# Kernel tuning notes

Hardware: AMD Instinct MI355X
Metric: run time of the kernel (lower is better)

The kernel has to match this reference:

```python
import jax, jax.numpy as jnp
import numpy as np

BOX_WARP = 1.0
TRIPLANE_DEPTH = 1
PLANES = jnp.array([[[1, 0, 0], [0, 1, 0], [0, 0, 1]],
                    [[1, 0, 0], [0, 0, 1], [0, 1, 0]],
                    [[0, 1, 0], [0, 0, 1], [1, 0, 0]]], dtype=jnp.float32)
INV_PLANES = jnp.linalg.inv(PLANES)  # [3,3,3]


def project_onto_planes(coords):
    # coords [N,M,3] -> projections [N*3, M, 3] (bmm with inverse plane axes)
    N, M, _ = coords.shape
    proj = jnp.einsum('nmc,pcd->npmd', coords, INV_PLANES)
    return proj.reshape(N * 3, M, 3)


def grid_sample_3d(feat, grid):
    # torch.nn.functional.grid_sample 5D, mode=bilinear(trilinear), padding_mode=zeros,
    # align_corners=False. feat [B,C,D,H,W], grid [B,M,3] with (x->W, y->H, z->D).
    B, C, D, H, W = feat.shape
    x = ((grid[..., 0] + 1.0) * W - 1.0) * 0.5
    y = ((grid[..., 1] + 1.0) * H - 1.0) * 0.5
    z = ((grid[..., 2] + 1.0) * D - 1.0) * 0.5
    x0f = jnp.floor(x); y0f = jnp.floor(y); z0f = jnp.floor(z)
    wx = x - x0f; wy = y - y0f; wz = z - z0f
    x0 = x0f.astype(jnp.int32); y0 = y0f.astype(jnp.int32); z0 = z0f.astype(jnp.int32)
    feat_flat = feat.reshape(B, C, D * H * W)

    def corner(zi, yi, xi, w):
        valid = ((zi >= 0) & (zi < D) & (yi >= 0) & (yi < H) & (xi >= 0) & (xi < W))
        idx = (jnp.clip(zi, 0, D - 1) * H + jnp.clip(yi, 0, H - 1)) * W + jnp.clip(xi, 0, W - 1)
        v = jnp.take_along_axis(feat_flat, idx[:, None, :], axis=2)  # [B,C,M]
        return v * (w * valid)[:, None, :]

    out = (corner(z0, y0, x0, (1 - wz) * (1 - wy) * (1 - wx))
           + corner(z0, y0, x0 + 1, (1 - wz) * (1 - wy) * wx)
           + corner(z0, y0 + 1, x0, (1 - wz) * wy * (1 - wx))
           + corner(z0, y0 + 1, x0 + 1, (1 - wz) * wy * wx)
           + corner(z0 + 1, y0, x0, wz * (1 - wy) * (1 - wx))
           + corner(z0 + 1, y0, x0 + 1, wz * (1 - wy) * wx)
           + corner(z0 + 1, y0 + 1, x0, wz * wy * (1 - wx))
           + corner(z0 + 1, y0 + 1, x0 + 1, wz * wy * wx))
    return out  # [B,C,M]


def sample_from_planes(plane_feats_list, coordinates):
    N, M, _ = coordinates.shape
    proj = project_onto_planes(coordinates * (2.0 / BOX_WARP))  # [N*3,M,3]
    out = None
    for pf in plane_feats_list:
        _, P, CD, H, W = pf.shape
        C = CD // TRIPLANE_DEPTH
        f = pf.reshape(N * 3, C, TRIPLANE_DEPTH, H, W)
        s = grid_sample_3d(f, proj)  # [N*3,C,M]
        s = s.reshape(N, 3, C, M).transpose(0, 1, 3, 2)  # [N,3,M,C]
        out = s if out is None else out + s
    return out / len(plane_feats_list)


def ray_march(colors, densities, depths):
    # MipRayMarcher2 (EG3D): midpoint sampling, softplus(d-1) activation, alpha compositing.
    deltas = depths[:, :, 1:] - depths[:, :, :-1]                    # [N,R,S-1,1]
    cmid = 0.5 * (colors[:, :, :-1] + colors[:, :, 1:])
    dmid = 0.5 * (densities[:, :, :-1] + densities[:, :, 1:])
    dmid = jax.nn.softplus(dmid - 1.0)
    alpha = 1.0 - jnp.exp(-dmid * deltas)                            # [N,R,S-1,1]
    shifted = jnp.concatenate([jnp.ones_like(alpha[:, :, :1]), 1.0 - alpha + 1e-10], axis=2)
    weights = alpha * jnp.cumprod(shifted, axis=2)[:, :, :-1]
    rgb = jnp.sum(weights * cmid, axis=2)                            # [N,R,3]
    return rgb


def setup_inputs() -> dict:
    key = jax.random.key(0)
    ks = jax.random.split(key, 6)
    N, C = 4, 32
    R, S = 4096, 48
    M = R * S
    plane_lo = jax.random.normal(ks[0], (N, 3, C, 256, 256), jnp.float32) * 0.1
    plane_hi = jax.random.normal(ks[1], (N, 3, C, 512, 512), jnp.float32) * 0.1
    coordinates = jax.random.uniform(ks[2], (N, M, 3), jnp.float32, -0.45, 0.45)
    depths = 2.25 + 1.2 * jnp.sort(jax.random.uniform(ks[3], (N, R, S, 1), jnp.float32), axis=2)
    w_sigma = jax.random.normal(ks[4], (C, 1), jnp.float32) * 0.1
    w_rgb = jax.random.normal(ks[5], (C, 3), jnp.float32) * 0.1
    return {"plane_lo": plane_lo, "plane_hi": plane_hi, "coordinates": coordinates,
            "depths": depths, "w_sigma": w_sigma, "w_rgb": w_rgb}


def reference(plane_lo, plane_hi, coordinates, depths, w_sigma, w_rgb):
    N, R, S, _ = depths.shape
    feats = sample_from_planes([plane_lo, plane_hi], coordinates).mean(axis=1)  # [N,M,C]
    sigma = feats @ w_sigma                                                      # [N,M,1]
    rgb = jax.nn.sigmoid(feats @ w_rgb)                                          # [N,M,3]
    return ray_march(rgb.reshape(N, R, S, 3), sigma.reshape(N, R, S, 1), depths)
```

## Files before the change

### kernel.cpp

```cpp
#include <hip/hip_runtime.h>
#include <hip/hip_bf16.h>
#include <cstdint>

#define N_IMG 4
#define C_CH 32
#define R_RAYS 4096
#define S_SAMP 48
#define M_PTS (R_RAYS * S_SAMP)

typedef float f32x4 __attribute__((ext_vector_type(4)));
typedef unsigned int u32x4 __attribute__((ext_vector_type(4)));

__device__ __forceinline__ unsigned f2bf(float f) {
  __hip_bfloat16 h = __float2bfloat16(f);
  return (unsigned)*reinterpret_cast<unsigned short*>(&h);
}
__device__ __forceinline__ float bflo(unsigned u) { return __uint_as_float(u << 16); }
__device__ __forceinline__ float bfhi(unsigned u) { return __uint_as_float(u & 0xffff0000u); }

#define LO_BLOCKS 768
#define HI_BLOCKS 3072

__global__ __launch_bounds__(256) void project_planes(
    const float* __restrict__ lo, const float* __restrict__ hi,
    const float* __restrict__ w_sigma, const float* __restrict__ w_rgb,
    uint4* __restrict__ lo_out, uint4* __restrict__ hi_out) {
  __shared__ float sw[4 * C_CH];
  int t = threadIdx.x;
  if (t < C_CH) sw[t * 4] = w_sigma[t];
  if (t < 3 * C_CH) sw[(t / 3) * 4 + 1 + (t % 3)] = w_rgb[t];
  __syncthreads();

  int bid = blockIdx.x;
  const float* in;
  uint4* out;
  int logW, g, c0, c1;
  if (bid < LO_BLOCKS) {
    in = lo; out = lo_out; logW = 8; g = bid * 256 + t; c0 = 11; c1 = 244;
  } else {
    in = hi; out = hi_out; logW = 9; g = (bid - LO_BLOCKS) * 256 + t; c0 = 24; c1 = 488;
  }
  int W = 1 << logW;
  int hw = (g * 4) & ((W * W) - 1);
  int np = (g * 4) >> (2 * logW);
  int h = hw >> logW, w = hw & (W - 1);
  if (h < c0 || h > c1 || (w + 3) < c0 || w > c1) return;

  const float* base = in + ((size_t)np << (5 + 2 * logW)) + hw;
  f32x4 as = 0.f, ar = 0.f, ag = 0.f, ab = 0.f;
#pragma unroll
  for (int c = 0; c < C_CH; ++c) {
    f32x4 f;
    __builtin_memcpy(&f, base + ((size_t)c << (2 * logW)), 16);
    as += f * sw[c * 4 + 0];
    ar += f * sw[c * 4 + 1];
    ag += f * sw[c * 4 + 2];
    ab += f * sw[c * 4 + 3];
  }
  uint4 o0, o1;
  o0.x = f2bf(as.x) | (f2bf(ar.x) << 16);
  o0.y = f2bf(ag.x) | (f2bf(ab.x) << 16);
  o0.z = f2bf(as.y) | (f2bf(ar.y) << 16);
  o0.w = f2bf(ag.y) | (f2bf(ab.y) << 16);
  o1.x = f2bf(as.z) | (f2bf(ar.z) << 16);
  o1.y = f2bf(ag.z) | (f2bf(ab.z) << 16);
  o1.z = f2bf(as.w) | (f2bf(ar.w) << 16);
  o1.w = f2bf(ag.w) | (f2bf(ab.w) << 16);
  out[g * 2 + 0] = o0;
  out[g * 2 + 1] = o1;
}

__global__ __launch_bounds__(256) void gather_pts(
    const float* __restrict__ coords,
    const uint2* __restrict__ lo_p,
    const uint2* __restrict__ hi_p,
    float4* __restrict__ pts)
{
  int idx = blockIdx.x * 256 + threadIdx.x;
  int n = idx / M_PTS;

  float X = coords[idx * 3 + 0] * 2.f;
  float Y = coords[idx * 3 + 1] * 2.f;
  float Z = coords[idx * 3 + 2] * 2.f;

  float acc0 = 0.f, acc1 = 0.f, acc2 = 0.f, acc3 = 0.f;
  const float gxs[3] = {X, X, Y};
  const float gys[3] = {Y, Z, Z};
  const float gzs[3] = {Z, Y, X};

#pragma unroll
  for (int p = 0; p < 3; ++p) {
    float wz = (1.f - 0.5f * fabsf(gzs[p])) * (1.f / 6.f);
#pragma unroll
    for (int lev = 0; lev < 2; ++lev) {
      const int logW = lev ? 9 : 8;
      const int W = 1 << logW;
      const uint2* pl = lev ? hi_p : lo_p;
      float xf = ((gxs[p] + 1.f) * (float)W - 1.f) * 0.5f;
      float yf = ((gys[p] + 1.f) * (float)W - 1.f) * 0.5f;
      float x0f = floorf(xf), y0f = floorf(yf);
      float fx = xf - x0f, fy = yf - y0f;
      int x0 = (int)x0f, y0 = (int)y0f;
      x0 = min(max(x0, 0), W - 2);
      y0 = min(max(y0, 0), W - 2);
      int base = ((((n * 3 + p) << logW) + y0) << logW) + x0;
      u32x4 r0, r1;
      __builtin_memcpy(&r0, pl + base, 16);
      __builtin_memcpy(&r1, pl + base + W, 16);
      float w00 = wz * (1.f - fy) * (1.f - fx);
      float w01 = wz * (1.f - fy) * fx;
      float w10 = wz * fy * (1.f - fx);
      float w11 = wz * fy * fx;
      acc0 += w00 * bflo(r0.x) + w01 * bflo(r0.z) + w10 * bflo(r1.x) + w11 * bflo(r1.z);
      acc1 += w00 * bfhi(r0.x) + w01 * bfhi(r0.z) + w10 * bfhi(r1.x) + w11 * bfhi(r1.z);
      acc2 += w00 * bflo(r0.y) + w01 * bflo(r0.w) + w10 * bflo(r1.y) + w11 * bflo(r1.w);
      acc3 += w00 * bfhi(r0.y) + w01 * bfhi(r0.w) + w10 * bfhi(r1.y) + w11 * bfhi(r1.w);
    }
  }

  float4 o;
  o.x = 1.f / (1.f + __expf(-acc1));
  o.y = 1.f / (1.f + __expf(-acc2));
  o.z = 1.f / (1.f + __expf(-acc3));
  o.w = acc0;
  pts[idx] = o;
}

__global__ __launch_bounds__(256) void ray_march_k(
    const float4* __restrict__ pts, const float* __restrict__ depths,
    float* __restrict__ out) {
  int t = blockIdx.x * 256 + threadIdx.x;
  const float4* p = pts + (size_t)t * S_SAMP;
  const float* d = depths + (size_t)t * S_SAMP;

  float4 prev = p[0];
  float dprev = d[0];
  float T = 1.f, accR = 0.f, accG = 0.f, accB = 0.f;
#pragma unroll 4
  for (int i = 1; i < S_SAMP; ++i) {
    float4 cur = p[i];
    float dcur = d[i];
    float delta = dcur - dprev;
    float cr = 0.5f * (prev.x + cur.x);
    float cg = 0.5f * (prev.y + cur.y);
    float cb = 0.5f * (prev.z + cur.z);
    float dm = 0.5f * (prev.w + cur.w) - 1.f;
    float sp = fmaxf(dm, 0.f) + log1pf(__expf(-fabsf(dm)));
    float a = 1.f - __expf(-sp * delta);
    float w = a * T;
    accR += w * cr; accG += w * cg; accB += w * cb;
    T *= (1.f - a + 1e-10f);
    prev = cur; dprev = dcur;
  }
  out[t * 3 + 0] = accR;
  out[t * 3 + 1] = accG;
  out[t * 3 + 2] = accB;
}

extern "C" void kernel_launch(void* const* d_in, const int* in_sizes, int n_in,
                              void* d_out, int out_size, void* d_ws, size_t ws_size,
                              hipStream_t stream) {
  const float* plane_lo = (const float*)d_in[0];
  const float* plane_hi = (const float*)d_in[1];
  const float* coords   = (const float*)d_in[2];
  const float* depths   = (const float*)d_in[3];
  const float* w_sigma  = (const float*)d_in[4];
  const float* w_rgb    = (const float*)d_in[5];

  const size_t LO_TEX = (size_t)12 * 256 * 256;
  const size_t HI_TEX = (size_t)12 * 512 * 512;
  char* ws = (char*)d_ws;
  uint2* lo_p = (uint2*)ws;
  uint2* hi_p = (uint2*)(ws + LO_TEX * 8);
  float4* pts = (float4*)(ws + (LO_TEX + HI_TEX) * 8);

  project_planes<<<LO_BLOCKS + HI_BLOCKS, 256, 0, stream>>>(
      plane_lo, plane_hi, w_sigma, w_rgb, (uint4*)lo_p, (uint4*)hi_p);

  gather_pts<<<(N_IMG * M_PTS) / 256, 256, 0, stream>>>(
      coords, lo_p, hi_p, pts);

  ray_march_k<<<(N_IMG * R_RAYS) / 256, 256, 0, stream>>>(
      pts, depths, (float*)d_out);
}
```

Measured before the change: 180.2 us.

## Split point gather into per-level passes with bf16 intermediate

Splits the gather kernel into a low-resolution pass and a high-resolution pass, so each pass touches only one projected texture. The partial sums go through a bf16 workspace buffer. Each pass processes two points per thread, uses nontemporal loads and stores, and interleaves blocks across images. The ray-march block size drops to 64 so more CUs get work. This adds an extra intermediate write and read, reads the coordinates twice, and loses some precision from rounding the partial sums to bf16.

```diff
diff --git a/kernel.cpp b/kernel.cpp
--- a/kernel.cpp
+++ b/kernel.cpp
@@ -7,9 +7,11 @@
 #define R_RAYS 4096
 #define S_SAMP 48
 #define M_PTS (R_RAYS * S_SAMP)
+#define TOTAL_PTS (N_IMG * M_PTS)
 
 typedef float f32x4 __attribute__((ext_vector_type(4)));
 typedef unsigned int u32x4 __attribute__((ext_vector_type(4)));
+typedef unsigned int u32x2 __attribute__((ext_vector_type(2)));
 
 __device__ __forceinline__ unsigned f2bf(float f) {
   __hip_bfloat16 h = __float2bfloat16(f);
@@ -70,66 +72,113 @@
   out[g * 2 + 1] = o1;
 }
 
-__global__ __launch_bounds__(256) void gather_pts(
+__device__ __forceinline__ void surf_accum(
+    const uint2* __restrict__ tex, int pb, int logW,
+    float gx, float gy, float wz, float* acc) {
+  const int W = 1 << logW;
+  float xf = ((gx + 1.f) * (float)W - 1.f) * 0.5f;
+  float yf = ((gy + 1.f) * (float)W - 1.f) * 0.5f;
+  float x0f = floorf(xf), y0f = floorf(yf);
+  float fx = xf - x0f, fy = yf - y0f;
+  int x0 = (int)x0f, y0 = (int)y0f;
+  x0 = min(max(x0, 0), W - 2);
+  y0 = min(max(y0, 0), W - 2);
+  int base = pb + (y0 << logW) + x0;
+  u32x4 r0, r1;
+  __builtin_memcpy(&r0, tex + base, 16);
+  __builtin_memcpy(&r1, tex + base + W, 16);
+  float w00 = wz * (1.f - fy) * (1.f - fx);
+  float w01 = wz * (1.f - fy) * fx;
+  float w10 = wz * fy * (1.f - fx);
+  float w11 = wz * fy * fx;
+  acc[0] += w00 * bflo(r0.x) + w01 * bflo(r0.z) + w10 * bflo(r1.x) + w11 * bflo(r1.z);
+  acc[1] += w00 * bfhi(r0.x) + w01 * bfhi(r0.z) + w10 * bfhi(r1.x) + w11 * bfhi(r1.z);
+  acc[2] += w00 * bflo(r0.y) + w01 * bflo(r0.w) + w10 * bflo(r1.y) + w11 * bflo(r1.w);
+  acc[3] += w00 * bfhi(r0.y) + w01 * bfhi(r0.w) + w10 * bfhi(r1.y) + w11 * bfhi(r1.w);
+}
+
+__global__ __launch_bounds__(256) void gather_lo(
     const float* __restrict__ coords,
     const uint2* __restrict__ lo_p,
+    unsigned* __restrict__ mid) {
+  int bid = blockIdx.x;
+  int n = (bid & 7) >> 1;
+  int blk = ((bid >> 3) << 1) + (bid & 1);
+  int base = n * M_PTS + blk * 512 + threadIdx.x;
+
+  float acc[2][4];
+#pragma unroll
+  for (int q = 0; q < 2; ++q) {
+    int idx = base + q * 256;
+    float X = __builtin_nontemporal_load(coords + idx * 3 + 0) * 2.f;
+    float Y = __builtin_nontemporal_load(coords + idx * 3 + 1) * 2.f;
+    float Z = __builtin_nontemporal_load(coords + idx * 3 + 2) * 2.f;
+    acc[q][0] = 0.f; acc[q][1] = 0.f; acc[q][2] = 0.f; acc[q][3] = 0.f;
+    const float gxs[3] = {X, X, Y};
+    const float gys[3] = {Y, Z, Z};
+    const float gzs[3] = {Z, Y, X};
+#pragma unroll
+    for (int p = 0; p < 3; ++p) {
+      float wz = (1.f - 0.5f * fabsf(gzs[p])) * (1.f / 6.f);
+      surf_accum(lo_p, (n * 3 + p) << 16, 8, gxs[p], gys[p], wz, acc[q]);
+    }
+  }
+#pragma unroll
+  for (int q = 0; q < 2; ++q) {
+    u32x2 m;
+    m.x = f2bf(acc[q][0]) | (f2bf(acc[q][1]) << 16);
+    m.y = f2bf(acc[q][2]) | (f2bf(acc[q][3]) << 16);
+    __builtin_nontemporal_store(
+        m, reinterpret_cast<u32x2*>(mid) + base + q * 256);
+  }
+}
+
+__global__ __launch_bounds__(256) void gather_hi(
+    const float* __restrict__ coords,
     const uint2* __restrict__ hi_p,
-    float4* __restrict__ pts)
-{
-  int idx = blockIdx.x * 256 + threadIdx.x;
-  int n = idx / M_PTS;
-
-  float X = coords[idx * 3 + 0] * 2.f;
-  float Y = coords[idx * 3 + 1] * 2.f;
-  float Z = coords[idx * 3 + 2] * 2.f;
-
-  float acc0 = 0.f, acc1 = 0.f, acc2 = 0.f, acc3 = 0.f;
-  const float gxs[3] = {X, X, Y};
-  const float gys[3] = {Y, Z, Z};
-  const float gzs[3] = {Z, Y, X};
-
-#pragma unroll
-  for (int p = 0; p < 3; ++p) {
-    float wz = (1.f - 0.5f * fabsf(gzs[p])) * (1.f / 6.f);
-#pragma unroll
-    for (int lev = 0; lev < 2; ++lev) {
-      const int logW = lev ? 9 : 8;
-      const int W = 1 << logW;
-      const uint2* pl = lev ? hi_p : lo_p;
-      float xf = ((gxs[p] + 1.f) * (float)W - 1.f) * 0.5f;
-      float yf = ((gys[p] + 1.f) * (float)W - 1.f) * 0.5f;
-      float x0f = floorf(xf), y0f = floorf(yf);
-      float fx = xf - x0f, fy = yf - y0f;
-      int x0 = (int)x0f, y0 = (int)y0f;
-      x0 = min(max(x0, 0), W - 2);
-      y0 = min(max(y0, 0), W - 2);
-      int base = ((((n * 3 + p) << logW) + y0) << logW) + x0;
-      u32x4 r0, r1;
-      __builtin_memcpy(&r0, pl + base, 16);
-      __builtin_memcpy(&r1, pl + base + W, 16);
-      float w00 = wz * (1.f - fy) * (1.f - fx);
-      float w01 = wz * (1.f - fy) * fx;
-      float w10 = wz * fy * (1.f - fx);
-      float w11 = wz * fy * fx;
-      acc0 += w00 * bflo(r0.x) + w01 * bflo(r0.z) + w10 * bflo(r1.x) + w11 * bflo(r1.z);
-      acc1 += w00 * bfhi(r0.x) + w01 * bfhi(r0.z) + w10 * bfhi(r1.x) + w11 * bfhi(r1.z);
-      acc2 += w00 * bflo(r0.y) + w01 * bflo(r0.w) + w10 * bflo(r1.y) + w11 * bflo(r1.w);
-      acc3 += w00 * bfhi(r0.y) + w01 * bfhi(r0.w) + w10 * bfhi(r1.y) + w11 * bfhi(r1.w);
+    const unsigned* __restrict__ mid,
+    float* __restrict__ pts) {
+  int bid = blockIdx.x;
+  int n = (bid & 7) >> 1;
+  int blk = ((bid >> 3) << 1) + (bid & 1);
+  int base = n * M_PTS + blk * 512 + threadIdx.x;
+
+  float acc[2][4];
+#pragma unroll
+  for (int q = 0; q < 2; ++q) {
+    int idx = base + q * 256;
+    u32x2 m = __builtin_nontemporal_load(
+        reinterpret_cast<const u32x2*>(mid) + idx);
+    float X = __builtin_nontemporal_load(coords + idx * 3 + 0) * 2.f;
+    float Y = __builtin_nontemporal_load(coords + idx * 3 + 1) * 2.f;
+    float Z = __builtin_nontemporal_load(coords + idx * 3 + 2) * 2.f;
+    acc[q][0] = bflo(m.x); acc[q][1] = bfhi(m.x);
+    acc[q][2] = bflo(m.y); acc[q][3] = bfhi(m.y);
+    const float gxs[3] = {X, X, Y};
+    const float gys[3] = {Y, Z, Z};
+    const float gzs[3] = {Z, Y, X};
+#pragma unroll
+    for (int p = 0; p < 3; ++p) {
+      float wz = (1.f - 0.5f * fabsf(gzs[p])) * (1.f / 6.f);
+      surf_accum(hi_p, (n * 3 + p) << 18, 9, gxs[p], gys[p], wz, acc[q]);
     }
   }
-
-  float4 o;
-  o.x = 1.f / (1.f + __expf(-acc1));
-  o.y = 1.f / (1.f + __expf(-acc2));
-  o.z = 1.f / (1.f + __expf(-acc3));
-  o.w = acc0;
-  pts[idx] = o;
-}
-
-__global__ __launch_bounds__(256) void ray_march_k(
+#pragma unroll
+  for (int q = 0; q < 2; ++q) {
+    f32x4 o;
+    o.x = 1.f / (1.f + __expf(-acc[q][1]));
+    o.y = 1.f / (1.f + __expf(-acc[q][2]));
+    o.z = 1.f / (1.f + __expf(-acc[q][3]));
+    o.w = acc[q][0];
+    __builtin_nontemporal_store(
+        o, reinterpret_cast<f32x4*>(pts) + base + q * 256);
+  }
+}
+
+__global__ __launch_bounds__(64) void ray_march_k(
     const float4* __restrict__ pts, const float* __restrict__ depths,
     float* __restrict__ out) {
-  int t = blockIdx.x * 256 + threadIdx.x;
+  int t = blockIdx.x * 64 + threadIdx.x;
   const float4* p = pts + (size_t)t * S_SAMP;
   const float* d = depths + (size_t)t * S_SAMP;
 
@@ -172,14 +221,16 @@
   char* ws = (char*)d_ws;
   uint2* lo_p = (uint2*)ws;
   uint2* hi_p = (uint2*)(ws + LO_TEX * 8);
-  float4* pts = (float4*)(ws + (LO_TEX + HI_TEX) * 8);
+  unsigned* mid = (unsigned*)(ws + (LO_TEX + HI_TEX) * 8);
+  float* pts = (float*)(ws + (LO_TEX + HI_TEX) * 8
+                           + (size_t)TOTAL_PTS * 8);
 
   project_planes<<<LO_BLOCKS + HI_BLOCKS, 256, 0, stream>>>(
       plane_lo, plane_hi, w_sigma, w_rgb, (uint4*)lo_p, (uint4*)hi_p);
 
-  gather_pts<<<(N_IMG * M_PTS) / 256, 256, 0, stream>>>(
-      coords, lo_p, hi_p, pts);
-
-  ray_march_k<<<(N_IMG * R_RAYS) / 256, 256, 0, stream>>>(
-      pts, depths, (float*)d_out);
-}
+  gather_lo<<<TOTAL_PTS / 512, 256, 0, stream>>>(coords, lo_p, mid);
+  gather_hi<<<TOTAL_PTS / 512, 256, 0, stream>>>(coords, hi_p, mid, pts);
+
+  ray_march_k<<<(N_IMG * R_RAYS) / 64, 64, 0, stream>>>(
+      (const float4*)pts, depths, (float*)d_out);
+}
```

After: 172.7 us. -4.2%, faster.
